# Optimization experiments

Measured on AMD Instinct MI355X. Metric: run time of the kernel, lower is better.

The kernel has to match this reference:

```python
import jax, jax.numpy as jnp
import numpy as np

N = 20000        # total nodes
E = 240000       # directed edges (avg in-degree 12); self-loops appended in reference
G = 50           # graphs in the batch
NPG = N // G     # nodes per graph
TD = 768         # text embedding dim
HC = 64          # hidden_channels
H = 8            # attention heads for conv1..conv3 (conv4 uses 1 head)
FD = 3 * HC * H + HC  # JK cat dim for num_layers=4
NEG = 0.2        # GATv2 leaky_relu negative slope
EPS = 1e-5       # GraphNorm eps


def setup_inputs() -> dict:
    key = jax.random.key(0)
    ks = iter(jax.random.split(key, 64))

    def w(shape, s=0.05):
        return jax.random.normal(next(ks), shape, dtype=jnp.float32) * s

    z = lambda *s: jnp.zeros(s, jnp.float32)
    o = lambda *s: jnp.ones(s, jnp.float32)

    inp = {
        'x': w((N, TD), 1.0),
        'edge_index': jax.random.randint(next(ks), (2, E), 0, N, dtype=jnp.int32),
        'batch': jnp.arange(N, dtype=jnp.int32) // NPG,
        'ptr': jnp.arange(G + 1, dtype=jnp.int32) * NPG,
        'tp_w': w((TD, HC)), 'tp_b': z(HC),
        'lin_w': w((FD, 1), 0.005), 'lin_b': z(1),
    }
    # GATv2Conv params: lin_l (source), lin_r (target), att, output bias
    for name, ind, heads, concat in [('c1', HC, H, True), ('c2', HC * H, H, True),
                                     ('c3', HC * H, H, True), ('c4', HC * H, 1, False)]:
        inp[name + '_wl'] = w((ind, heads * HC)); inp[name + '_bl'] = z(heads * HC)
        inp[name + '_wr'] = w((ind, heads * HC)); inp[name + '_br'] = z(heads * HC)
        inp[name + '_att'] = w((heads, HC))
        inp[name + '_bias'] = z(heads * HC if concat else HC)
    # GraphNorm params: weight, bias, mean_scale
    for name, d in [('n1', HC * H), ('n2', HC * H), ('n3', HC * H), ('n4', HC)]:
        inp[name + '_w'] = o(d); inp[name + '_b'] = z(d); inp[name + '_ms'] = o(d)
    return inp


def _gatv2(x, src, dst, wl, bl, wr, br, att, bias, heads, concat):
    # GATv2: e_ij = att . leaky_relu(W_l x_j + W_r x_i); alpha = softmax over in-neighbors of i
    xl = (x @ wl + bl).reshape(N, heads, HC)
    xr = (x @ wr + br).reshape(N, heads, HC)
    e = jax.nn.leaky_relu(xl[src] + xr[dst], NEG)           # [E', H, C]
    logit = jnp.einsum('ehc,hc->eh', e, att)                # [E', H]
    m = jax.ops.segment_max(logit, dst, num_segments=N)     # stable scatter-softmax
    p = jnp.exp(logit - m[dst])
    alpha = p / jax.ops.segment_sum(p, dst, num_segments=N)[dst]
    out = jax.ops.segment_sum(xl[src] * alpha[..., None], dst, num_segments=N)
    out = out.reshape(N, heads * HC) if concat else out.mean(axis=1)
    return out + bias


def _gnorm(x, batch, w, b, ms):
    # PyG GraphNorm: per-graph mean (scaled by mean_scale), per-graph std
    cnt = jax.ops.segment_sum(jnp.ones((N,), x.dtype), batch, num_segments=G)[:, None]
    mean = jax.ops.segment_sum(x, batch, num_segments=G) / cnt
    cen = x - ms * mean[batch]
    var = jax.ops.segment_sum(cen * cen, batch, num_segments=G) / cnt
    return w * cen / jnp.sqrt(var + EPS)[batch] + b


def reference(x, tp_w, tp_b,
              c1_wl, c1_bl, c1_wr, c1_br, c1_att, c1_bias,
              c2_wl, c2_bl, c2_wr, c2_br, c2_att, c2_bias,
              c3_wl, c3_bl, c3_wr, c3_br, c3_att, c3_bias,
              c4_wl, c4_bl, c4_wr, c4_br, c4_att, c4_bias,
              n1_w, n1_b, n1_ms, n2_w, n2_b, n2_ms,
              n3_w, n3_b, n3_ms, n4_w, n4_b, n4_ms,
              lin_w, lin_b, edge_index, batch, ptr):
    sl = jnp.arange(N, dtype=edge_index.dtype)
    src = jnp.concatenate([edge_index[0], sl])  # add_self_loops=True
    dst = jnp.concatenate([edge_index[1], sl])

    h = x @ tp_w + tp_b                          # text_proj (dropout = identity in eval)
    h = _gatv2(h, src, dst, c1_wl, c1_bl, c1_wr, c1_br, c1_att, c1_bias, H, True)
    h = jax.nn.elu(_gnorm(h, batch, n1_w, n1_b, n1_ms))
    xs = [h]
    h2 = _gatv2(h, src, dst, c2_wl, c2_bl, c2_wr, c2_br, c2_att, c2_bias, H, True)
    h = jax.nn.elu(_gnorm(h2 + h, batch, n2_w, n2_b, n2_ms))
    xs.append(h)
    h3 = _gatv2(h, src, dst, c3_wl, c3_bl, c3_wr, c3_br, c3_att, c3_bias, H, True)
    h = jax.nn.elu(_gnorm(h3 + h, batch, n3_w, n3_b, n3_ms))
    xs.append(h)
    h = _gnorm(_gatv2(h, src, dst, c4_wl, c4_bl, c4_wr, c4_br, c4_att, c4_bias, 1, False),
               batch, n4_w, n4_b, n4_ms)
    xs.append(h)

    xcat = jnp.concatenate(xs, axis=1)           # JumpingKnowledge cat -> [N, FD]
    out = xcat[ptr[:-1]] @ lin_w + lin_b         # summary node per graph -> [G, 1]
    return out.squeeze(-1)                       # num_classes==2 -> squeeze
```

## Files before the change

kernel.cpp:

```cpp
#include <hip/hip_runtime.h>
#include <hip/hip_bf16.h>

#define NEG_SLOPE 0.2f
#define EPSI 1e-5f

typedef __attribute__((ext_vector_type(8))) short bf16x8;
typedef __attribute__((ext_vector_type(4))) float f32x4;

__device__ __forceinline__ float wred_sum(float v){
#pragma unroll
  for (int o = 32; o > 0; o >>= 1) v += __shfl_xor(v, o);
  return v;
}

__device__ __forceinline__ unsigned short f2bf(float f){
  __hip_bfloat16 h = __float2bfloat16(f);
  return *reinterpret_cast<unsigned short*>(&h);
}
__device__ __forceinline__ float bf2f(unsigned short u){
  return __uint_as_float((unsigned int)u << 16);
}

__device__ __forceinline__ void gload16(const void* g, void* l){
  __builtin_amdgcn_global_load_lds((const __attribute__((address_space(1))) unsigned int*)g,
                                   (__attribute__((address_space(3))) unsigned int*)l, 16, 0, 0);
}

__global__ __launch_bounds__(256) void k_count(const int* __restrict__ ei, int* __restrict__ deg,
                                               int E, int EP){
  int e = blockIdx.x * 256 + threadIdx.x;
  if (e >= EP) return;
  int d = (e < E) ? ei[E + e] : (e - E);
  atomicAdd(&deg[d], 1);
}

__global__ __launch_bounds__(256) void k_scan(const int* __restrict__ deg, int* __restrict__ rowptr, int n){
  __shared__ int part[256];
  int t = threadIdx.x;
  int L = (n + 255) / 256;
  int lo = t * L, hi = min(lo + L, n);
  int s = 0;
  for (int i = lo; i < hi; i++) s += deg[i];
  part[t] = s;
  __syncthreads();
  if (t == 0){
    int acc = 0;
    for (int i = 0; i < 256; i++){ int v = part[i]; part[i] = acc; acc += v; }
  }
  __syncthreads();
  int acc = part[t];
  for (int i = lo; i < hi; i++){ rowptr[i] = acc; acc += deg[i]; }
  if (t == 255) rowptr[n] = acc;
}

__global__ __launch_bounds__(256) void k_copy(const int* __restrict__ a, int* __restrict__ b, int n){
  int i = blockIdx.x * 256 + threadIdx.x;
  if (i < n) b[i] = a[i];
}

__global__ __launch_bounds__(256) void k_fill(const int* __restrict__ ei, int* __restrict__ cursor,
                                              int* __restrict__ srcn, int E, int EP){
  int e = blockIdx.x * 256 + threadIdx.x;
  if (e >= EP) return;
  int s, d;
  if (e < E){ s = ei[e]; d = ei[E + e]; } else { s = d = e - E; }
  int pos = atomicAdd(&cursor[d], 1);
  srcn[pos] = s;
}

__global__ __launch_bounds__(256) void k_cvt_act(const float* __restrict__ in,
                                                 unsigned short* __restrict__ ob, int total4){
  int i = blockIdx.x * 256 + threadIdx.x;
  if (i >= total4) return;
  float4 v = ((const float4*)in)[i];
  ushort4 o;
  o.x = f2bf(v.x); o.y = f2bf(v.y); o.z = f2bf(v.z); o.w = f2bf(v.w);
  ((ushort4*)ob)[i] = o;
}

__global__ __launch_bounds__(256) void k_cvt_wt(const float* __restrict__ W,
                                                unsigned short* __restrict__ Wt,
                                                int K, int Ncol){
  __shared__ float t[32][33];
  int bx = blockIdx.x, by = blockIdx.y;
  int tx = threadIdx.x & 31, ty = threadIdx.x >> 5;
#pragma unroll
  for (int i = 0; i < 4; i++)
    t[ty + i * 8][tx] = W[(size_t)(by * 32 + ty + i * 8) * Ncol + bx * 32 + tx];
  __syncthreads();
#pragma unroll
  for (int i = 0; i < 4; i++)
    Wt[(size_t)(bx * 32 + ty + i * 8) * K + by * 32 + tx] = f2bf(t[tx][ty + i * 8]);
}

__global__ __launch_bounds__(64) void k_cat2(const float* __restrict__ a,
                                             const float* __restrict__ b,
                                             float* __restrict__ o){
  int i = threadIdx.x;
  o[i] = a[i];
  o[64 + i] = b[i];
}

template<int BN>
__global__ __launch_bounds__(256) void k_gemm_mfma_t(const unsigned short* __restrict__ A,
                                                     const unsigned short* __restrict__ Wt,
                                                     const float* __restrict__ bias,
                                                     unsigned short* __restrict__ Cb,
                                                     int M, int K, int Ncol){
  constexpr int NF = BN / 32;
  __shared__ unsigned short As[128 * 32];
  __shared__ unsigned short Bs[BN * 32];
  const int tid = threadIdx.x;
  const int w = tid >> 6, lane = tid & 63;
  const int wr = w >> 1, wc = w & 1;
  const int row0 = blockIdx.y * 128, col0 = blockIdx.x * BN;
  const int lr = lane & 15, lk = lane >> 4;
  const int swz = (lr >> 1) & 3;

  f32x4 acc[4][NF];
#pragma unroll
  for (int i = 0; i < 4; i++)
#pragma unroll
    for (int j = 0; j < NF; j++) acc[i][j] = (f32x4){0.f, 0.f, 0.f, 0.f};

  for (int k0 = 0; k0 < K; k0 += 32){
#pragma unroll
    for (int c = 0; c < 2; c++){
      int g = w * 128 + c * 64 + lane;
      int row = g >> 2, slot = g & 3;
      int kq = slot ^ ((row >> 1) & 3);
      int srow = row0 + row; if (srow >= M) srow = M - 1;
      gload16(&A[(size_t)srow * K + k0 + kq * 8], &As[(size_t)(w * 128 + c * 64) * 8]);
    }
#pragma unroll
    for (int c = 0; c < BN / 64; c++){
      int g = w * BN + c * 64 + lane;
      int col = g >> 2, slot = g & 3;
      int kq = slot ^ ((col >> 1) & 3);
      gload16(&Wt[(size_t)(col0 + col) * K + k0 + kq * 8], &Bs[(size_t)(w * BN + c * 64) * 8]);
    }
    __syncthreads();

    bf16x8 af[4], bf_[NF];
#pragma unroll
    for (int mi = 0; mi < 4; mi++){
      int rl = wr * 64 + mi * 16 + lr;
      af[mi] = *(const bf16x8*)&As[(rl * 4 + (lk ^ swz)) * 8];
    }
#pragma unroll
    for (int ni = 0; ni < NF; ni++){
      int cl = wc * (BN / 2) + ni * 16 + lr;
      bf_[ni] = *(const bf16x8*)&Bs[(cl * 4 + (lk ^ swz)) * 8];
    }
#pragma unroll
    for (int mi = 0; mi < 4; mi++)
#pragma unroll
      for (int ni = 0; ni < NF; ni++)
        acc[mi][ni] = __builtin_amdgcn_mfma_f32_16x16x32_bf16(af[mi], bf_[ni], acc[mi][ni], 0, 0, 0);
    __syncthreads();
  }

#pragma unroll
  for (int mi = 0; mi < 4; mi++){
#pragma unroll
    for (int ni = 0; ni < NF; ni++){
      int gc = col0 + wc * (BN / 2) + ni * 16 + lr;
      float bv = bias[gc];
#pragma unroll
      for (int r = 0; r < 4; r++){
        int gr = row0 + wr * 64 + mi * 16 + lk * 4 + r;
        if (gr < M) Cb[(size_t)gr * Ncol + gc] = f2bf(acc[mi][ni][r] + bv);
      }
    }
  }
}

__global__ __launch_bounds__(256) void k_gat_fused8(const unsigned short* __restrict__ xlb,
                                                    const unsigned short* __restrict__ xrb,
                                                    const float* __restrict__ att,
                                                    const int* __restrict__ rowptr,
                                                    const int* __restrict__ srcn,
                                                    const float* __restrict__ bias,
                                                    const float* __restrict__ res,
                                                    float* __restrict__ out,
                                                    int N){
  int node = (blockIdx.x * 256 + threadIdx.x) >> 6;
  int lane = threadIdx.x & 63;
  if (node >= N) return;
  float xr[8], av[8];
  {
    bf16x8 r8 = *(const bf16x8*)&xrb[(size_t)node * 512 + lane * 8];
    float4 a0 = *(const float4*)&att[lane * 8];
    float4 a1 = *(const float4*)&att[lane * 8 + 4];
#pragma unroll
    for (int j = 0; j < 8; j++) xr[j] = bf2f((unsigned short)r8[j]);
    av[0] = a0.x; av[1] = a0.y; av[2] = a0.z; av[3] = a0.w;
    av[4] = a1.x; av[5] = a1.y; av[6] = a1.z; av[7] = a1.w;
  }
  int e0 = rowptr[node], e1 = rowptr[node + 1];
  float m = -1e30f, s = 0.f;
  float acc[8] = {};
  for (int base = e0; base < e1; base += 64){
    int cnt = min(64, e1 - base);
    int sn = 0;
    if (lane < cnt) sn = srcn[base + lane];
    for (int k = 0; k < cnt; k++){
      int sk = __shfl(sn, k);
      bf16x8 v8 = *(const bf16x8*)&xlb[(size_t)sk * 512 + lane * 8];
      float v[8];
#pragma unroll
      for (int j = 0; j < 8; j++) v[j] = bf2f((unsigned short)v8[j]);
      float sum = 0.f;
#pragma unroll
      for (int j = 0; j < 8; j++){
        float t = v[j] + xr[j];
        t = t > 0.f ? t : NEG_SLOPE * t;
        sum += t * av[j];
      }
      sum += __shfl_xor(sum, 1);
      sum += __shfl_xor(sum, 2);
      sum += __shfl_xor(sum, 4);
      float mo = m;
      m = fmaxf(m, sum);
      float cs = __expf(mo - m);
      float p  = __expf(sum - m);
      s = s * cs + p;
#pragma unroll
      for (int j = 0; j < 8; j++) acc[j] = acc[j] * cs + p * v[j];
    }
  }
  float inv = 1.f / s;
  size_t o = (size_t)node * 512 + lane * 8;
  float4 bv0 = *(const float4*)&bias[lane * 8];
  float4 bv1 = *(const float4*)&bias[lane * 8 + 4];
  float4 r0 = make_float4(0.f, 0.f, 0.f, 0.f), r1 = make_float4(0.f, 0.f, 0.f, 0.f);
  if (res){ r0 = *(const float4*)&res[o]; r1 = *(const float4*)&res[o + 4]; }
  float4 o0, o1;
  o0.x = acc[0] * inv + bv0.x + r0.x;
  o0.y = acc[1] * inv + bv0.y + r0.y;
  o0.z = acc[2] * inv + bv0.z + r0.z;
  o0.w = acc[3] * inv + bv0.w + r0.w;
  o1.x = acc[4] * inv + bv1.x + r1.x;
  o1.y = acc[5] * inv + bv1.y + r1.y;
  o1.z = acc[6] * inv + bv1.z + r1.z;
  o1.w = acc[7] * inv + bv1.w + r1.w;
  *(float4*)&out[o] = o0;
  *(float4*)&out[o + 4] = o1;
}

__global__ __launch_bounds__(256) void k_gat_fused1(const unsigned short* __restrict__ xlr,
                                                    const float* __restrict__ att,
                                                    const int* __restrict__ rowptr,
                                                    const int* __restrict__ srcn,
                                                    const float* __restrict__ bias,
                                                    float* __restrict__ out,
                                                    int N){
  int node = (blockIdx.x * 256 + threadIdx.x) >> 6;
  int lane = threadIdx.x & 63;
  if (node >= N) return;
  float xrv = bf2f(xlr[(size_t)node * 128 + 64 + lane]);
  float attv = att[lane];
  int e0 = rowptr[node], e1 = rowptr[node + 1];
  float m = -1e30f, s = 0.f, acc = 0.f;
  for (int base = e0; base < e1; base += 64){
    int cnt = min(64, e1 - base);
    int sn = 0;
    if (lane < cnt) sn = srcn[base + lane];
    for (int k = 0; k < cnt; k++){
      int sk = __shfl(sn, k);
      float v = bf2f(xlr[(size_t)sk * 128 + lane]);
      float t = v + xrv;
      t = t > 0.f ? t : NEG_SLOPE * t;
      float sum = wred_sum(t * attv);
      float mo = m;
      m = fmaxf(m, sum);
      float cs = __expf(mo - m);
      float p  = __expf(sum - m);
      s = s * cs + p;
      acc = acc * cs + p * v;
    }
  }
  out[(size_t)node * 64 + lane] = acc / s + bias[lane];
}

#define NCHUNK 16
__global__ __launch_bounds__(256) void k_gnorm_stats(const float* __restrict__ y,
                                                     const int* __restrict__ ptrg,
                                                     float* __restrict__ psum,
                                                     float* __restrict__ psq,
                                                     int OD){
  int g = blockIdx.x, chunk = blockIdx.z;
  int lane = threadIdx.x & 63, sub = threadIdx.x >> 6;
  int c = blockIdx.y * 64 + lane;
  int lo = ptrg[g], hi = ptrg[g + 1], len = hi - lo;
  int c0 = lo + (len * chunk) / NCHUNK, c1 = lo + (len * (chunk + 1)) / NCHUNK;
  float s = 0.f, q = 0.f;
  for (int i = c0 + sub; i < c1; i += 4){
    float v = y[(size_t)i * OD + c];
    s += v; q += v * v;
  }
  __shared__ float sm[4][64], sq2[4][64];
  sm[sub][lane] = s; sq2[sub][lane] = q;
  __syncthreads();
  if (sub == 0){
    s = sm[0][lane] + sm[1][lane] + sm[2][lane] + sm[3][lane];
    q = sq2[0][lane] + sq2[1][lane] + sq2[2][lane] + sq2[3][lane];
    size_t o = (size_t)(g * NCHUNK + chunk) * OD + c;
    psum[o] = s; psq[o] = q;
  }
}

__global__ __launch_bounds__(256) void k_gnorm_coef(const float* __restrict__ psum,
                                                    const float* __restrict__ psq,
                                                    const float* __restrict__ w,
                                                    const float* __restrict__ b,
                                                    const float* __restrict__ ms,
                                                    const int* __restrict__ ptrg,
                                                    float* __restrict__ cA,
                                                    float* __restrict__ cC,
                                                    int OD){
  int g = blockIdx.x;
  int len = ptrg[g + 1] - ptrg[g];
  float inv_n = 1.f / (float)len;
  for (int c = threadIdx.x; c < OD; c += 256){
    float s = 0.f, q = 0.f;
    for (int k = 0; k < NCHUNK; k++){
      size_t o = (size_t)(g * NCHUNK + k) * OD + c;
      s += psum[o]; q += psq[o];
    }
    float mean = s * inv_n, ey2 = q * inv_n;
    float m = ms[c];
    float var = ey2 - mean * mean * (2.f * m - m * m);
    float inv = rsqrtf(var + EPSI);
    float A = w[c] * inv;
    cA[(size_t)g * OD + c] = A;
    cC[(size_t)g * OD + c] = b[c] - A * m * mean;
  }
}

__global__ __launch_bounds__(256) void k_gnorm_apply(const float* __restrict__ y,
                                                     const int* __restrict__ batch,
                                                     const float* __restrict__ cA,
                                                     const float* __restrict__ cC,
                                                     float* __restrict__ out,
                                                     unsigned short* __restrict__ outb,
                                                     int OD, int total4, int do_elu){
  int idx = blockIdx.x * 256 + threadIdx.x;
  if (idx >= total4) return;
  int od4 = OD >> 2;
  int node = idx / od4;
  int c = (idx - node * od4) << 2;
  int g = batch[node];
  float4 v = ((const float4*)y)[idx];
  float4 A = *(const float4*)&cA[(size_t)g * OD + c];
  float4 Cc = *(const float4*)&cC[(size_t)g * OD + c];
  float4 r;
  r.x = A.x * v.x + Cc.x;
  r.y = A.y * v.y + Cc.y;
  r.z = A.z * v.z + Cc.z;
  r.w = A.w * v.w + Cc.w;
  if (do_elu){
    r.x = r.x > 0.f ? r.x : expf(r.x) - 1.f;
    r.y = r.y > 0.f ? r.y : expf(r.y) - 1.f;
    r.z = r.z > 0.f ? r.z : expf(r.z) - 1.f;
    r.w = r.w > 0.f ? r.w : expf(r.w) - 1.f;
  }
  ((float4*)out)[idx] = r;
  if (outb){
    ushort4 ob;
    ob.x = f2bf(r.x); ob.y = f2bf(r.y); ob.z = f2bf(r.z); ob.w = f2bf(r.w);
    ((ushort4*)outb)[idx] = ob;
  }
}

__global__ __launch_bounds__(64) void k_extract(const float* __restrict__ srcb,
                                                float* __restrict__ cat,
                                                const int* __restrict__ ptrg,
                                                int OD, int off, int FD){
  int g = blockIdx.x;
  int c = blockIdx.y * 64 + threadIdx.x;
  cat[(size_t)g * FD + off + c] = srcb[(size_t)ptrg[g] * OD + c];
}

__global__ __launch_bounds__(256) void k_final(const float* __restrict__ cat,
                                               const float* __restrict__ lin_w,
                                               const float* __restrict__ lin_b,
                                               float* __restrict__ out, int FD){
  int g = blockIdx.x;
  float s = 0.f;
  for (int c = threadIdx.x; c < FD; c += 256) s += cat[(size_t)g * FD + c] * lin_w[c];
  s = wred_sum(s);
  __shared__ float sm[4];
  if ((threadIdx.x & 63) == 0) sm[threadIdx.x >> 6] = s;
  __syncthreads();
  if (threadIdx.x == 0) out[g] = sm[0] + sm[1] + sm[2] + sm[3] + lin_b[0];
}

extern "C" void kernel_launch(void* const* d_in, const int* in_sizes, int n_in,
                              void* d_out, int out_size, void* d_ws, size_t ws_size,
                              hipStream_t stream) {
  const int TD = 768, HC = 64, H = 8;
  const float* x     = (const float*)d_in[0];
  const int*   ei    = (const int*)d_in[1];
  const int*   batch = (const int*)d_in[2];
  const int*   ptrg  = (const int*)d_in[3];
  const float* tp_w  = (const float*)d_in[4];
  const float* tp_b  = (const float*)d_in[5];
  const float* lin_w = (const float*)d_in[6];
  const float* lin_b = (const float*)d_in[7];
  const float* cw[4][6];
  for (int l = 0; l < 4; l++)
    for (int j = 0; j < 6; j++) cw[l][j] = (const float*)d_in[8 + 6 * l + j];
  const float* nw[4][3];
  for (int l = 0; l < 4; l++)
    for (int j = 0; j < 3; j++) nw[l][j] = (const float*)d_in[32 + 3 * l + j];

  const int N  = in_sizes[0] / TD;
  const int E  = in_sizes[1] / 2;
  const int EP = E + N;
  const int G  = in_sizes[3] - 1;
  const int FD = 3 * HC * H + HC;

  char* wsp = (char*)d_ws;
  size_t off = 0;
  auto alloc = [&](size_t b) -> void* {
    void* p = wsp + off;
    off += (b + 255) & ~(size_t)255;
    return p;
  };
  float* tmpF  = (float*)alloc((size_t)N * 512 * 4);
  float* bufP  = (float*)alloc((size_t)N * 512 * 4);
  float* bufQ  = (float*)alloc((size_t)N * 512 * 4);
  unsigned short* xlb = (unsigned short*)alloc((size_t)N * 512 * 2);
  unsigned short* xrb = (unsigned short*)alloc((size_t)N * 512 * 2);
  unsigned short* actA = (unsigned short*)alloc((size_t)N * 512 * 2);
  unsigned short* actB = (unsigned short*)alloc((size_t)N * 512 * 2);
  unsigned short* h0h = (unsigned short*)alloc((size_t)N * 64 * 2);
  int*   rowptr= (int*)alloc((size_t)(N + 1) * 4);
  int*   cursor= (int*)alloc((size_t)N * 4);
  int*   srcn  = (int*)alloc((size_t)EP * 4);
  float* cat   = (float*)alloc((size_t)G * FD * 4);
  float* psum  = (float*)alloc((size_t)G * NCHUNK * 512 * 4);
  float* psq   = (float*)alloc((size_t)G * NCHUNK * 512 * 4);
  float* cA    = (float*)alloc((size_t)G * 512 * 4);
  float* cC    = (float*)alloc((size_t)G * 512 * 4);
  unsigned short* WtL = (unsigned short*)alloc((size_t)512 * 512 * 2);
  unsigned short* WtR = (unsigned short*)alloc((size_t)512 * 512 * 2);
  unsigned short* WtTP = (unsigned short*)alloc((size_t)64 * 768 * 2);
  unsigned short* Wt4  = (unsigned short*)alloc((size_t)128 * 512 * 2);
  float* cbias4 = (float*)alloc(128 * 4);
  (void)ws_size; (void)n_in; (void)out_size;

  float* out = (float*)d_out;

  unsigned short* xbf   = xlb;
  unsigned short* xlr4b = xlb;
  float* agg4 = tmpF;
  float* out4 = tmpF + (size_t)N * 64;

  hipMemsetAsync(cursor, 0, (size_t)N * 4, stream);
  int eblk = (EP + 255) / 256;
  k_count<<<eblk, 256, 0, stream>>>(ei, cursor, E, EP);
  k_scan<<<1, 256, 0, stream>>>(cursor, rowptr, N);
  k_copy<<<(N + 255) / 256, 256, 0, stream>>>(rowptr, cursor, N);
  k_fill<<<eblk, 256, 0, stream>>>(ei, cursor, srcn, E, EP);

  const int mfmaRows = (N + 127) / 128;
  const int nodeBlocks = (N + 3) / 4;

  k_cvt_act<<<(N * TD / 4 + 255) / 256, 256, 0, stream>>>(x, xbf, N * TD / 4);
  k_cvt_wt<<<dim3(2, TD / 32), 256, 0, stream>>>(tp_w, WtTP, TD, 64);
  k_gemm_mfma_t<64><<<dim3(1, mfmaRows), 256, 0, stream>>>(xbf, WtTP, tp_b, h0h, N, TD, 64);

  auto layer8 = [&](const unsigned short* actbf, int Kin, int l, const float* res,
                    float* yout, unsigned short* youtb, int catoff){
    k_cvt_wt<<<dim3(16, Kin / 32), 256, 0, stream>>>(cw[l][0], WtL, Kin, 512);
    k_cvt_wt<<<dim3(16, Kin / 32), 256, 0, stream>>>(cw[l][2], WtR, Kin, 512);
    k_gemm_mfma_t<128><<<dim3(4, mfmaRows), 256, 0, stream>>>(actbf, WtL, cw[l][1], xlb, N, Kin, 512);
    k_gemm_mfma_t<128><<<dim3(4, mfmaRows), 256, 0, stream>>>(actbf, WtR, cw[l][3], xrb, N, Kin, 512);
    k_gat_fused8<<<nodeBlocks, 256, 0, stream>>>(xlb, xrb, cw[l][4], rowptr, srcn,
                                                 cw[l][5], res, tmpF, N);
    k_gnorm_stats<<<dim3(G, 8, NCHUNK), 256, 0, stream>>>(tmpF, ptrg, psum, psq, 512);
    k_gnorm_coef<<<G, 256, 0, stream>>>(psum, psq, nw[l][0], nw[l][1], nw[l][2], ptrg, cA, cC, 512);
    int total4 = N * 128;
    k_gnorm_apply<<<(total4 + 255) / 256, 256, 0, stream>>>(tmpF, batch, cA, cC, yout, youtb,
                                                            512, total4, 1);
    k_extract<<<dim3(G, 8), 64, 0, stream>>>(yout, cat, ptrg, 512, catoff, FD);
  };

  layer8(h0h,  64,  0, nullptr, bufP, actA, 0);
  layer8(actA, 512, 1, bufP,    bufQ, actB, 512);
  layer8(actB, 512, 2, bufQ,    bufP, actA, 1024);

  k_cvt_wt<<<dim3(2, 16), 256, 0, stream>>>(cw[3][0], Wt4, 512, 64);
  k_cvt_wt<<<dim3(2, 16), 256, 0, stream>>>(cw[3][2], Wt4 + (size_t)64 * 512, 512, 64);
  k_cat2<<<1, 64, 0, stream>>>(cw[3][1], cw[3][3], cbias4);
  k_gemm_mfma_t<64><<<dim3(2, mfmaRows), 256, 0, stream>>>(actA, Wt4, cbias4, xlr4b, N, 512, 128);
  k_gat_fused1<<<nodeBlocks, 256, 0, stream>>>(xlr4b, cw[3][4], rowptr, srcn,
                                               cw[3][5], agg4, N);
  k_gnorm_stats<<<dim3(G, 1, NCHUNK), 256, 0, stream>>>(agg4, ptrg, psum, psq, 64);
  k_gnorm_coef<<<G, 256, 0, stream>>>(psum, psq, nw[3][0], nw[3][1], nw[3][2], ptrg, cA, cC, 64);
  k_gnorm_apply<<<(N * 16 + 255) / 256, 256, 0, stream>>>(agg4, batch, cA, cC, out4, nullptr,
                                                          64, N * 16, 0);
  k_extract<<<dim3(G, 1), 64, 0, stream>>>(out4, cat, ptrg, 64, 1536, FD);

  k_final<<<G, 256, 0, stream>>>(cat, lin_w, lin_b, out, FD);
}
```

Baseline: 586.2 us.

## Merge L/R GEMMs, lazy softmax rescale, dual-edge unroll, bf16 residual path

Fuses the two per-layer projection GEMMs into one GEMM with 1024 output columns, writing interleaved xl/xr rows so the GAT kernel reads both from one buffer. The GAT aggregation kernels now handle two edges per iteration with two independent online-softmax accumulators, and only rescale when a logit exceeds the running max by a threshold, which removes most exp/rescale work. Residuals and layer outputs are kept in bf16 only, dropping the fp32 activation buffers and their writes. This trades some accuracy in the residual and JK-extracted features for less memory traffic, fewer launches and more instruction-level parallelism.

```diff
diff --git a/kernel.cpp b/kernel.cpp
--- a/kernel.cpp
+++ b/kernel.cpp
@@ -3,6 +3,7 @@
 
 #define NEG_SLOPE 0.2f
 #define EPSI 1e-5f
+#define THR 8.0f
 
 typedef __attribute__((ext_vector_type(8))) short bf16x8;
 typedef __attribute__((ext_vector_type(4))) float f32x4;
@@ -93,12 +94,12 @@
     Wt[(size_t)(bx * 32 + ty + i * 8) * K + by * 32 + tx] = f2bf(t[tx][ty + i * 8]);
 }
 
-__global__ __launch_bounds__(64) void k_cat2(const float* __restrict__ a,
-                                             const float* __restrict__ b,
-                                             float* __restrict__ o){
-  int i = threadIdx.x;
-  o[i] = a[i];
-  o[64 + i] = b[i];
+__global__ __launch_bounds__(256) void k_catb(const float* __restrict__ a,
+                                              const float* __restrict__ b,
+                                              float* __restrict__ o, int n){
+  int i = blockIdx.x * 256 + threadIdx.x;
+  if (i < n) o[i] = a[i];
+  else if (i < 2 * n) o[i] = b[i - n];
 }
 
 template<int BN>
@@ -175,13 +176,12 @@
   }
 }
 
-__global__ __launch_bounds__(256) void k_gat_fused8(const unsigned short* __restrict__ xlb,
-                                                    const unsigned short* __restrict__ xrb,
+__global__ __launch_bounds__(256) void k_gat_fused8(const unsigned short* __restrict__ xlrb,
                                                     const float* __restrict__ att,
                                                     const int* __restrict__ rowptr,
                                                     const int* __restrict__ srcn,
                                                     const float* __restrict__ bias,
-                                                    const float* __restrict__ res,
+                                                    const unsigned short* __restrict__ resb,
                                                     float* __restrict__ out,
                                                     int N){
   int node = (blockIdx.x * 256 + threadIdx.x) >> 6;
@@ -189,7 +189,7 @@
   if (node >= N) return;
   float xr[8], av[8];
   {
-    bf16x8 r8 = *(const bf16x8*)&xrb[(size_t)node * 512 + lane * 8];
+    bf16x8 r8 = *(const bf16x8*)&xlrb[(size_t)node * 1024 + 512 + lane * 8];
     float4 a0 = *(const float4*)&att[lane * 8];
     float4 a1 = *(const float4*)&att[lane * 8 + 4];
 #pragma unroll
@@ -198,52 +198,111 @@
     av[4] = a1.x; av[5] = a1.y; av[6] = a1.z; av[7] = a1.w;
   }
   int e0 = rowptr[node], e1 = rowptr[node + 1];
-  float m = -1e30f, s = 0.f;
-  float acc[8] = {};
+  float m0 = -1e30f, s0 = 0.f, m1 = -1e30f, s1 = 0.f;
+  float acc0[8] = {}, acc1[8] = {};
+
   for (int base = e0; base < e1; base += 64){
     int cnt = min(64, e1 - base);
     int sn = 0;
     if (lane < cnt) sn = srcn[base + lane];
-    for (int k = 0; k < cnt; k++){
-      int sk = __shfl(sn, k);
-      bf16x8 v8 = *(const bf16x8*)&xlb[(size_t)sk * 512 + lane * 8];
-      float v[8];
-#pragma unroll
-      for (int j = 0; j < 8; j++) v[j] = bf2f((unsigned short)v8[j]);
-      float sum = 0.f;
+    int k = 0;
+    for (; k + 1 < cnt; k += 2){
+      int ska = __shfl(sn, k);
+      int skb = __shfl(sn, k + 1);
+      bf16x8 va8 = *(const bf16x8*)&xlrb[(size_t)ska * 1024 + lane * 8];
+      bf16x8 vb8 = *(const bf16x8*)&xlrb[(size_t)skb * 1024 + lane * 8];
+      float va[8], vb[8];
+#pragma unroll
+      for (int j = 0; j < 8; j++){ va[j] = bf2f((unsigned short)va8[j]); vb[j] = bf2f((unsigned short)vb8[j]); }
+      float suma = 0.f, sumb = 0.f;
 #pragma unroll
       for (int j = 0; j < 8; j++){
-        float t = v[j] + xr[j];
-        t = t > 0.f ? t : NEG_SLOPE * t;
-        sum += t * av[j];
-      }
-      sum += __shfl_xor(sum, 1);
-      sum += __shfl_xor(sum, 2);
-      sum += __shfl_xor(sum, 4);
-      float mo = m;
-      m = fmaxf(m, sum);
-      float cs = __expf(mo - m);
-      float p  = __expf(sum - m);
-      s = s * cs + p;
-#pragma unroll
-      for (int j = 0; j < 8; j++) acc[j] = acc[j] * cs + p * v[j];
-    }
-  }
+        float ta = va[j] + xr[j]; ta = ta > 0.f ? ta : NEG_SLOPE * ta; suma += ta * av[j];
+        float tb = vb[j] + xr[j]; tb = tb > 0.f ? tb : NEG_SLOPE * tb; sumb += tb * av[j];
+      }
+      suma += __shfl_xor(suma, 1); sumb += __shfl_xor(sumb, 1);
+      suma += __shfl_xor(suma, 2); sumb += __shfl_xor(sumb, 2);
+      suma += __shfl_xor(suma, 4); sumb += __shfl_xor(sumb, 4);
+      if (__builtin_expect(__any(suma > m0 + THR), 0)){
+        float mn = fmaxf(m0, suma);
+        float cs = __expf(m0 - mn);
+        float p  = __expf(suma - mn);
+        s0 = s0 * cs + p;
+#pragma unroll
+        for (int j = 0; j < 8; j++) acc0[j] = acc0[j] * cs + p * va[j];
+        m0 = mn;
+      } else {
+        float p = __expf(suma - m0);
+        s0 += p;
+#pragma unroll
+        for (int j = 0; j < 8; j++) acc0[j] += p * va[j];
+      }
+      if (__builtin_expect(__any(sumb > m1 + THR), 0)){
+        float mn = fmaxf(m1, sumb);
+        float cs = __expf(m1 - mn);
+        float p  = __expf(sumb - mn);
+        s1 = s1 * cs + p;
+#pragma unroll
+        for (int j = 0; j < 8; j++) acc1[j] = acc1[j] * cs + p * vb[j];
+        m1 = mn;
+      } else {
+        float p = __expf(sumb - m1);
+        s1 += p;
+#pragma unroll
+        for (int j = 0; j < 8; j++) acc1[j] += p * vb[j];
+      }
+    }
+    if (k < cnt){
+      int ska = __shfl(sn, k);
+      bf16x8 va8 = *(const bf16x8*)&xlrb[(size_t)ska * 1024 + lane * 8];
+      float va[8];
+#pragma unroll
+      for (int j = 0; j < 8; j++) va[j] = bf2f((unsigned short)va8[j]);
+      float suma = 0.f;
+#pragma unroll
+      for (int j = 0; j < 8; j++){
+        float ta = va[j] + xr[j]; ta = ta > 0.f ? ta : NEG_SLOPE * ta; suma += ta * av[j];
+      }
+      suma += __shfl_xor(suma, 1);
+      suma += __shfl_xor(suma, 2);
+      suma += __shfl_xor(suma, 4);
+      if (__builtin_expect(__any(suma > m0 + THR), 0)){
+        float mn = fmaxf(m0, suma);
+        float cs = __expf(m0 - mn);
+        float p  = __expf(suma - mn);
+        s0 = s0 * cs + p;
+#pragma unroll
+        for (int j = 0; j < 8; j++) acc0[j] = acc0[j] * cs + p * va[j];
+        m0 = mn;
+      } else {
+        float p = __expf(suma - m0);
+        s0 += p;
+#pragma unroll
+        for (int j = 0; j < 8; j++) acc0[j] += p * va[j];
+      }
+    }
+  }
+  float m = fmaxf(m0, m1);
+  float c0 = __expf(m0 - m), c1 = __expf(m1 - m);
+  float s = s0 * c0 + s1 * c1;
   float inv = 1.f / s;
   size_t o = (size_t)node * 512 + lane * 8;
   float4 bv0 = *(const float4*)&bias[lane * 8];
   float4 bv1 = *(const float4*)&bias[lane * 8 + 4];
-  float4 r0 = make_float4(0.f, 0.f, 0.f, 0.f), r1 = make_float4(0.f, 0.f, 0.f, 0.f);
-  if (res){ r0 = *(const float4*)&res[o]; r1 = *(const float4*)&res[o + 4]; }
+  float rr[8] = {};
+  if (resb){
+    bf16x8 r8 = *(const bf16x8*)&resb[o];
+#pragma unroll
+    for (int j = 0; j < 8; j++) rr[j] = bf2f((unsigned short)r8[j]);
+  }
+  float bb[8] = {bv0.x, bv0.y, bv0.z, bv0.w, bv1.x, bv1.y, bv1.z, bv1.w};
   float4 o0, o1;
-  o0.x = acc[0] * inv + bv0.x + r0.x;
-  o0.y = acc[1] * inv + bv0.y + r0.y;
-  o0.z = acc[2] * inv + bv0.z + r0.z;
-  o0.w = acc[3] * inv + bv0.w + r0.w;
-  o1.x = acc[4] * inv + bv1.x + r1.x;
-  o1.y = acc[5] * inv + bv1.y + r1.y;
-  o1.z = acc[6] * inv + bv1.z + r1.z;
-  o1.w = acc[7] * inv + bv1.w + r1.w;
+  float res8[8];
+#pragma unroll
+  for (int j = 0; j < 8; j++)
+    res8[j] = (acc0[j] * c0 + acc1[j] * c1) * inv + bb[j] + rr[j];
+  o0.x = res8[0]; o0.y = res8[1]; o0.z = res8[2]; o0.w = res8[3];
+  o1.x = res8[4]; o1.y = res8[5]; o1.z = res8[6]; o1.w = res8[7];
   *(float4*)&out[o] = o0;
   *(float4*)&out[o + 4] = o1;
 }
@@ -272,12 +331,18 @@
       float t = v + xrv;
       t = t > 0.f ? t : NEG_SLOPE * t;
       float sum = wred_sum(t * attv);
-      float mo = m;
-      m = fmaxf(m, sum);
-      float cs = __expf(mo - m);
-      float p  = __expf(sum - m);
-      s = s * cs + p;
-      acc = acc * cs + p * v;
+      if (sum > m + THR){
+        float mn = fmaxf(m, sum);
+        float cs = __expf(m - mn);
+        float p  = __expf(sum - mn);
+        s = s * cs + p;
+        acc = acc * cs + p * v;
+        m = mn;
+      } else {
+        float p = __expf(sum - m);
+        s += p;
+        acc += p * v;
+      }
     }
   }
   out[(size_t)node * 64 + lane] = acc / s + bias[lane];
@@ -342,7 +407,6 @@
                                                      const int* __restrict__ batch,
                                                      const float* __restrict__ cA,
                                                      const float* __restrict__ cC,
-                                                     float* __restrict__ out,
                                                      unsigned short* __restrict__ outb,
                                                      int OD, int total4, int do_elu){
   int idx = blockIdx.x * 256 + threadIdx.x;
@@ -365,21 +429,18 @@
     r.z = r.z > 0.f ? r.z : expf(r.z) - 1.f;
     r.w = r.w > 0.f ? r.w : expf(r.w) - 1.f;
   }
-  ((float4*)out)[idx] = r;
-  if (outb){
-    ushort4 ob;
-    ob.x = f2bf(r.x); ob.y = f2bf(r.y); ob.z = f2bf(r.z); ob.w = f2bf(r.w);
-    ((ushort4*)outb)[idx] = ob;
-  }
-}
-
-__global__ __launch_bounds__(64) void k_extract(const float* __restrict__ srcb,
+  ushort4 ob;
+  ob.x = f2bf(r.x); ob.y = f2bf(r.y); ob.z = f2bf(r.z); ob.w = f2bf(r.w);
+  ((ushort4*)outb)[idx] = ob;
+}
+
+__global__ __launch_bounds__(64) void k_extract(const unsigned short* __restrict__ srcb,
                                                 float* __restrict__ cat,
                                                 const int* __restrict__ ptrg,
                                                 int OD, int off, int FD){
   int g = blockIdx.x;
   int c = blockIdx.y * 64 + threadIdx.x;
-  cat[(size_t)g * FD + off + c] = srcb[(size_t)ptrg[g] * OD + c];
+  cat[(size_t)g * FD + off + c] = bf2f(srcb[(size_t)ptrg[g] * OD + c]);
 }
 
 __global__ __launch_bounds__(256) void k_final(const float* __restrict__ cat,
@@ -429,13 +490,9 @@
     return p;
   };
   float* tmpF  = (float*)alloc((size_t)N * 512 * 4);
-  float* bufP  = (float*)alloc((size_t)N * 512 * 4);
-  float* bufQ  = (float*)alloc((size_t)N * 512 * 4);
-  unsigned short* xlb = (unsigned short*)alloc((size_t)N * 512 * 2);
-  unsigned short* xrb = (unsigned short*)alloc((size_t)N * 512 * 2);
+  unsigned short* xlrb = (unsigned short*)alloc((size_t)N * 1024 * 2);
   unsigned short* actA = (unsigned short*)alloc((size_t)N * 512 * 2);
-  unsigned short* actB = (unsigned short*)alloc((size_t)N * 512 * 2);
-  unsigned short* h0h = (unsigned short*)alloc((size_t)N * 64 * 2);
+  unsigned short* h0h  = (unsigned short*)alloc((size_t)N * 64 * 2);
   int*   rowptr= (int*)alloc((size_t)(N + 1) * 4);
   int*   cursor= (int*)alloc((size_t)N * 4);
   int*   srcn  = (int*)alloc((size_t)EP * 4);
@@ -444,19 +501,17 @@
   float* psq   = (float*)alloc((size_t)G * NCHUNK * 512 * 4);
   float* cA    = (float*)alloc((size_t)G * 512 * 4);
   float* cC    = (float*)alloc((size_t)G * 512 * 4);
-  unsigned short* WtL = (unsigned short*)alloc((size_t)512 * 512 * 2);
-  unsigned short* WtR = (unsigned short*)alloc((size_t)512 * 512 * 2);
+  unsigned short* WtLR = (unsigned short*)alloc((size_t)1024 * 512 * 2);
   unsigned short* WtTP = (unsigned short*)alloc((size_t)64 * 768 * 2);
   unsigned short* Wt4  = (unsigned short*)alloc((size_t)128 * 512 * 2);
-  float* cbias4 = (float*)alloc(128 * 4);
+  float* cbias = (float*)alloc(1024 * 4);
   (void)ws_size; (void)n_in; (void)out_size;
 
   float* out = (float*)d_out;
 
-  unsigned short* xbf   = xlb;
-  unsigned short* xlr4b = xlb;
+  unsigned short* xbf   = xlrb;
+  unsigned short* xlr4b = xlrb;
   float* agg4 = tmpF;
-  float* out4 = tmpF + (size_t)N * 64;
 
   hipMemsetAsync(cursor, 0, (size_t)N * 4, stream);
   int eblk = (EP + 255) / 256;
@@ -472,37 +527,37 @@
   k_cvt_wt<<<dim3(2, TD / 32), 256, 0, stream>>>(tp_w, WtTP, TD, 64);
   k_gemm_mfma_t<64><<<dim3(1, mfmaRows), 256, 0, stream>>>(xbf, WtTP, tp_b, h0h, N, TD, 64);
 
-  auto layer8 = [&](const unsigned short* actbf, int Kin, int l, const float* res,
-                    float* yout, unsigned short* youtb, int catoff){
-    k_cvt_wt<<<dim3(16, Kin / 32), 256, 0, stream>>>(cw[l][0], WtL, Kin, 512);
-    k_cvt_wt<<<dim3(16, Kin / 32), 256, 0, stream>>>(cw[l][2], WtR, Kin, 512);
-    k_gemm_mfma_t<128><<<dim3(4, mfmaRows), 256, 0, stream>>>(actbf, WtL, cw[l][1], xlb, N, Kin, 512);
-    k_gemm_mfma_t<128><<<dim3(4, mfmaRows), 256, 0, stream>>>(actbf, WtR, cw[l][3], xrb, N, Kin, 512);
-    k_gat_fused8<<<nodeBlocks, 256, 0, stream>>>(xlb, xrb, cw[l][4], rowptr, srcn,
-                                                 cw[l][5], res, tmpF, N);
+  auto layer8 = [&](const unsigned short* actbf, int Kin, int l,
+                    const unsigned short* resb, unsigned short* youtb, int catoff){
+    k_cvt_wt<<<dim3(16, Kin / 32), 256, 0, stream>>>(cw[l][0], WtLR, Kin, 512);
+    k_cvt_wt<<<dim3(16, Kin / 32), 256, 0, stream>>>(cw[l][2], WtLR + (size_t)512 * Kin, Kin, 512);
+    k_catb<<<4, 256, 0, stream>>>(cw[l][1], cw[l][3], cbias, 512);
+    k_gemm_mfma_t<128><<<dim3(8, mfmaRows), 256, 0, stream>>>(actbf, WtLR, cbias, xlrb, N, Kin, 1024);
+    k_gat_fused8<<<nodeBlocks, 256, 0, stream>>>(xlrb, cw[l][4], rowptr, srcn,
+                                                 cw[l][5], resb, tmpF, N);
     k_gnorm_stats<<<dim3(G, 8, NCHUNK), 256, 0, stream>>>(tmpF, ptrg, psum, psq, 512);
     k_gnorm_coef<<<G, 256, 0, stream>>>(psum, psq, nw[l][0], nw[l][1], nw[l][2], ptrg, cA, cC, 512);
     int total4 = N * 128;
-    k_gnorm_apply<<<(total4 + 255) / 256, 256, 0, stream>>>(tmpF, batch, cA, cC, yout, youtb,
+    k_gnorm_apply<<<(total4 + 255) / 256, 256, 0, stream>>>(tmpF, batch, cA, cC, youtb,
                                                             512, total4, 1);
-    k_extract<<<dim3(G, 8), 64, 0, stream>>>(yout, cat, ptrg, 512, catoff, FD);
+    k_extract<<<dim3(G, 8), 64, 0, stream>>>(youtb, cat, ptrg, 512, catoff, FD);
   };
 
-  layer8(h0h,  64,  0, nullptr, bufP, actA, 0);
-  layer8(actA, 512, 1, bufP,    bufQ, actB, 512);
-  layer8(actB, 512, 2, bufQ,    bufP, actA, 1024);
+  layer8(h0h,  64,  0, nullptr, actA, 0);
+  layer8(actA, 512, 1, actA,    actA, 512);
+  layer8(actA, 512, 2, actA,    actA, 1024);
 
   k_cvt_wt<<<dim3(2, 16), 256, 0, stream>>>(cw[3][0], Wt4, 512, 64);
   k_cvt_wt<<<dim3(2, 16), 256, 0, stream>>>(cw[3][2], Wt4 + (size_t)64 * 512, 512, 64);
-  k_cat2<<<1, 64, 0, stream>>>(cw[3][1], cw[3][3], cbias4);
-  k_gemm_mfma_t<64><<<dim3(2, mfmaRows), 256, 0, stream>>>(actA, Wt4, cbias4, xlr4b, N, 512, 128);
+  k_catb<<<1, 256, 0, stream>>>(cw[3][1], cw[3][3], cbias, 64);
+  k_gemm_mfma_t<64><<<dim3(2, mfmaRows), 256, 0, stream>>>(actA, Wt4, cbias, xlr4b, N, 512, 128);
   k_gat_fused1<<<nodeBlocks, 256, 0, stream>>>(xlr4b, cw[3][4], rowptr, srcn,
                                                cw[3][5], agg4, N);
   k_gnorm_stats<<<dim3(G, 1, NCHUNK), 256, 0, stream>>>(agg4, ptrg, psum, psq, 64);
   k_gnorm_coef<<<G, 256, 0, stream>>>(psum, psq, nw[3][0], nw[3][1], nw[3][2], ptrg, cA, cC, 64);
-  k_gnorm_apply<<<(N * 16 + 255) / 256, 256, 0, stream>>>(agg4, batch, cA, cC, out4, nullptr,
+  k_gnorm_apply<<<(N * 16 + 255) / 256, 256, 0, stream>>>(agg4, batch, cA, cC, h0h,
                                                           64, N * 16, 0);
-  k_extract<<<dim3(G, 1), 64, 0, stream>>>(out4, cat, ptrg, 64, 1536, FD);
+  k_extract<<<dim3(G, 1), 64, 0, stream>>>(h0h, cat, ptrg, 64, 1536, FD);
 
   k_final<<<G, 256, 0, stream>>>(cat, lin_w, lin_b, out, FD);
 }
```

Measured after the change: 551.2 us. 1.06x faster.
